# Performance work log

Hardware: AMD Instinct MI355X
Metric: run time of the kernel (lower is better)

The kernel has to match this reference:

```python
import jax, jax.numpy as jnp
import numpy as np

B, S, D, FF, E = 4, 2048, 2048, 8192, 2


def setup_inputs() -> dict:
    key = jax.random.key(0)
    k0, k1, k2, k3, k4 = jax.random.split(key, 5)
    s = 0.02  # init scale for weights
    return {
        "hidden_states": jax.random.normal(k0, (B, S, D), jnp.float32),
        "gate_w": jax.random.normal(k1, (E, D), jnp.float32) * s,   # router Linear weight
        "w_gate": jax.random.normal(k2, (E, FF, D), jnp.float32) * s,  # per-expert gate_proj
        "w_up": jax.random.normal(k3, (E, FF, D), jnp.float32) * s,    # per-expert up_proj
        "w_down": jax.random.normal(k4, (E, D, FF), jnp.float32) * s,  # per-expert down_proj
    }


def reference(hidden_states, gate_w, w_gate, w_up, w_down):
    b, s, d = hidden_states.shape
    x = hidden_states.reshape(-1, d)                      # [T, D], T = B*S
    logits = x @ gate_w.T                                  # [T, E]
    probs = jax.nn.softmax(logits.astype(jnp.float32), axis=-1)
    sel = jnp.argmax(probs, axis=-1)                       # top-1 expert per token
    top_w = jnp.take_along_axis(probs, sel[:, None], axis=-1)  # [T, 1] routing weight
    onehot = jax.nn.one_hot(sel, gate_w.shape[0], dtype=x.dtype)  # [T, E]
    # Dense per-expert MistralMLP: down(silu(gate(x)) * up(x)); top-1 combine via one-hot mask.
    g = jnp.einsum('td,efd->etf', x, w_gate)               # [E, T, FF]
    u = jnp.einsum('td,efd->etf', x, w_up)                 # [E, T, FF]
    h = jax.nn.silu(g) * u
    y = jnp.einsum('etf,edf->etd', h, w_down)              # [E, T, D]
    out = jnp.einsum('etd,te->td', y, onehot * top_w)      # weighted scatter-combine
    return out.reshape(b, s, d)
```

## Files before the change

kernel.cpp:

```cpp
#include <hip/hip_runtime.h>
#include <hip/hip_bf16.h>

#define T_TOK   8192
#define D_DIM   2048
#define FF_DIM  8192
#define PADT    8448

#define C_CNT0 0
#define C_CNT1 1
#define C_CUR0 2
#define C_BASE1 4
#define C_PTOT 5

typedef __attribute__((ext_vector_type(4))) float f32x4;
typedef __attribute__((ext_vector_type(8))) short short8;

__device__ __forceinline__ unsigned short f2bf(float f) {
  union { __hip_bfloat16 b; unsigned short u; } cv;
  cv.b = __float2bfloat16(f);
  return cv.u;
}

__device__ __forceinline__ void gload16(const void* g, void* l) {
  __builtin_amdgcn_global_load_lds(
      (const __attribute__((address_space(1))) void*)g,
      (__attribute__((address_space(3))) void*)l,
      16, 0, 0);
}

__global__ __launch_bounds__(256) void cvt_kernel(const float4* __restrict__ src,
                                                  ushort4* __restrict__ dst, int n4) {
  int i = blockIdx.x * blockDim.x + threadIdx.x;
  if (i < n4) {
    float4 v = src[i];
    dst[i] = make_ushort4(f2bf(v.x), f2bf(v.y), f2bf(v.z), f2bf(v.w));
  }
}

__global__ __launch_bounds__(256) void init_kernel(int* __restrict__ ctrl,
                                                   int* __restrict__ perm) {
  int i = blockIdx.x * blockDim.x + threadIdx.x;
  if (i < 8) ctrl[i] = 0;
  if (i < PADT) perm[i] = -1;
}

__global__ __launch_bounds__(256) void router_kernel(const float* __restrict__ x,
                                                     const float* __restrict__ gw,
                                                     int* __restrict__ sel,
                                                     float* __restrict__ topw,
                                                     int* __restrict__ ctrl) {
  const int w = threadIdx.x >> 6, l = threadIdx.x & 63;
  const int t = blockIdx.x * 4 + w;
  const float4* xr = (const float4*)(x + (size_t)t * D_DIM);
  const float4* g0 = (const float4*)gw;
  const float4* g1 = (const float4*)(gw + D_DIM);
  float d0 = 0.f, d1 = 0.f;
#pragma unroll
  for (int i = 0; i < 8; i++) {
    float4 v = xr[i * 64 + l];
    float4 a = g0[i * 64 + l];
    float4 b = g1[i * 64 + l];
    d0 += v.x * a.x + v.y * a.y + v.z * a.z + v.w * a.w;
    d1 += v.x * b.x + v.y * b.y + v.z * b.z + v.w * b.w;
  }
#pragma unroll
  for (int s = 32; s; s >>= 1) {
    d0 += __shfl_xor(d0, s);
    d1 += __shfl_xor(d1, s);
  }
  if (l == 0) {
    int e = (d1 > d0) ? 1 : 0;
    float dd = fabsf(d1 - d0);
    sel[t] = e;
    topw[t] = 1.f / (1.f + expf(-dd));
    atomicAdd(&ctrl[e], 1);
  }
}

__global__ void setup_kernel(int* __restrict__ ctrl) {
  if (threadIdx.x == 0) {
    int c0 = ctrl[C_CNT0], c1 = ctrl[C_CNT1];
    int b1 = ((c0 + 127) >> 7) << 7;
    ctrl[C_BASE1] = b1;
    ctrl[C_PTOT] = b1 + (((c1 + 127) >> 7) << 7);
  }
}

__global__ __launch_bounds__(256) void scatter_kernel(const int* __restrict__ sel,
                                                      int* __restrict__ ctrl,
                                                      int* __restrict__ perm) {
  int t = blockIdx.x * blockDim.x + threadIdx.x;
  int e = sel[t];
  int base = e ? ctrl[C_BASE1] : 0;
  int pos = base + atomicAdd(&ctrl[C_CUR0 + e], 1);
  perm[pos] = t;
}

__global__ __launch_bounds__(256) void gather_kernel(const float* __restrict__ x,
                                                     const int* __restrict__ perm,
                                                     const float* __restrict__ topw,
                                                     ushort* __restrict__ Xg,
                                                     float* __restrict__ twg) {
  const int w = threadIdx.x >> 6, l = threadIdx.x & 63;
  const int pos = blockIdx.x * 4 + w;
  const int t = perm[pos];
  if (l == 0) twg[pos] = (t >= 0) ? topw[t] : 0.f;
  ushort4* dst = (ushort4*)(Xg + (size_t)pos * D_DIM);
  if (t >= 0) {
    const float4* src = (const float4*)(x + (size_t)t * D_DIM);
#pragma unroll
    for (int i = 0; i < 8; i++) {
      float4 v = src[i * 64 + l];
      dst[i * 64 + l] = make_ushort4(f2bf(v.x), f2bf(v.y), f2bf(v.z), f2bf(v.w));
    }
  } else {
    ushort4 z = make_ushort4(0, 0, 0, 0);
#pragma unroll
    for (int i = 0; i < 8; i++) dst[i * 64 + l] = z;
  }
}

__global__ __launch_bounds__(256, 2) void gemm1_kernel(const ushort* __restrict__ Xg,
                                                       const ushort* __restrict__ Wg,
                                                       const ushort* __restrict__ Wu,
                                                       ushort* __restrict__ H,
                                                       const int* __restrict__ ctrl) {
  __shared__ ushort As[128 * 32];
  __shared__ ushort Bgs[128 * 32];
  __shared__ ushort Bus[128 * 32];

  const int row0 = blockIdx.x * 128;
  if (row0 >= ctrl[C_PTOT]) return;
  const int e = (row0 >= ctrl[C_BASE1]) ? 1 : 0;
  const int tn = blockIdx.y;

  const int tid = threadIdx.x;
  const int w = tid >> 6, l = tid & 63;
  const int wr = w >> 1, wc = w & 1;

  const ushort* A  = Xg + (size_t)row0 * D_DIM;
  const ushort* Bg = Wg + ((size_t)e * FF_DIM + (size_t)tn * 128) * D_DIM;
  const ushort* Bu = Wu + ((size_t)e * FF_DIM + (size_t)tn * 128) * D_DIM;

  const int q0 = w * 2, q1 = q0 + 1;
  const int scol = (l & 3) * 8;
  const ushort* a0  = A  + (size_t)(q0 * 16 + (l >> 2)) * D_DIM + scol;
  const ushort* a1  = A  + (size_t)(q1 * 16 + (l >> 2)) * D_DIM + scol;
  const ushort* bg0 = Bg + (size_t)(q0 * 16 + (l >> 2)) * D_DIM + scol;
  const ushort* bg1 = Bg + (size_t)(q1 * 16 + (l >> 2)) * D_DIM + scol;
  const ushort* bu0 = Bu + (size_t)(q0 * 16 + (l >> 2)) * D_DIM + scol;
  const ushort* bu1 = Bu + (size_t)(q1 * 16 + (l >> 2)) * D_DIM + scol;
  ushort* lA0 = &As [q0 * 512];
  ushort* lA1 = &As [q1 * 512];
  ushort* lG0 = &Bgs[q0 * 512];
  ushort* lG1 = &Bgs[q1 * 512];
  ushort* lU0 = &Bus[q0 * 512];
  ushort* lU1 = &Bus[q1 * 512];

  f32x4 accg[4][4] = {};
  f32x4 accu[4][4] = {};

  const int fr = l & 15, fk = (l >> 4) * 8;

  for (int k0 = 0; k0 < D_DIM; k0 += 32) {
    gload16(a0 + k0, lA0);
    gload16(a1 + k0, lA1);
    gload16(bg0 + k0, lG0);
    gload16(bg1 + k0, lG1);
    gload16(bu0 + k0, lU0);
    gload16(bu1 + k0, lU1);
    __syncthreads();
    short8 a[4], bg[4], bu[4];
#pragma unroll
    for (int i = 0; i < 4; i++) a[i]  = *(const short8*)&As [(wr * 64 + i * 16 + fr) * 32 + fk];
#pragma unroll
    for (int j = 0; j < 4; j++) bg[j] = *(const short8*)&Bgs[(wc * 64 + j * 16 + fr) * 32 + fk];
#pragma unroll
    for (int j = 0; j < 4; j++) bu[j] = *(const short8*)&Bus[(wc * 64 + j * 16 + fr) * 32 + fk];
#pragma unroll
    for (int i = 0; i < 4; i++)
#pragma unroll
      for (int j = 0; j < 4; j++) {
        accg[i][j] = __builtin_amdgcn_mfma_f32_16x16x32_bf16(a[i], bg[j], accg[i][j], 0, 0, 0);
        accu[i][j] = __builtin_amdgcn_mfma_f32_16x16x32_bf16(a[i], bu[j], accu[i][j], 0, 0, 0);
      }
    __syncthreads();
  }

  const int m4 = (l >> 4) * 4;
#pragma unroll
  for (int i = 0; i < 4; i++) {
#pragma unroll
    for (int r = 0; r < 4; r++) {
      size_t hrow = (size_t)(row0 + wr * 64 + i * 16 + m4 + r) * FF_DIM + (size_t)tn * 128 + wc * 64;
#pragma unroll
      for (int j = 0; j < 4; j++) {
        float g = accg[i][j][r], u = accu[i][j][r];
        float h = (g / (1.f + __expf(-g))) * u;
        H[hrow + j * 16 + fr] = f2bf(h);
      }
    }
  }
}

__global__ __launch_bounds__(256, 2) void gemm2_kernel(const ushort* __restrict__ H,
                                                       const ushort* __restrict__ Wd,
                                                       const int* __restrict__ perm,
                                                       const float* __restrict__ twg,
                                                       float* __restrict__ out,
                                                       const int* __restrict__ ctrl) {
  __shared__ ushort As[128 * 32];
  __shared__ ushort Bs[128 * 32];

  const int row0 = blockIdx.x * 128;
  if (row0 >= ctrl[C_PTOT]) return;
  const int e = (row0 >= ctrl[C_BASE1]) ? 1 : 0;
  const int tn = blockIdx.y;

  const int tid = threadIdx.x;
  const int w = tid >> 6, l = tid & 63;
  const int wr = w >> 1, wc = w & 1;

  const ushort* A = H  + (size_t)row0 * FF_DIM;
  const ushort* B = Wd + ((size_t)e * D_DIM + (size_t)tn * 128) * FF_DIM;

  const int q0 = w * 2, q1 = q0 + 1;
  const int scol = (l & 3) * 8;
  const ushort* a0 = A + (size_t)(q0 * 16 + (l >> 2)) * FF_DIM + scol;
  const ushort* a1 = A + (size_t)(q1 * 16 + (l >> 2)) * FF_DIM + scol;
  const ushort* b0 = B + (size_t)(q0 * 16 + (l >> 2)) * FF_DIM + scol;
  const ushort* b1 = B + (size_t)(q1 * 16 + (l >> 2)) * FF_DIM + scol;
  ushort* lA0 = &As[q0 * 512];
  ushort* lA1 = &As[q1 * 512];
  ushort* lB0 = &Bs[q0 * 512];
  ushort* lB1 = &Bs[q1 * 512];

  f32x4 acc[4][4] = {};
  const int fr = l & 15, fk = (l >> 4) * 8;

  for (int k0 = 0; k0 < FF_DIM; k0 += 32) {
    gload16(a0 + k0, lA0);
    gload16(a1 + k0, lA1);
    gload16(b0 + k0, lB0);
    gload16(b1 + k0, lB1);
    __syncthreads();
    short8 a[4], b[4];
#pragma unroll
    for (int i = 0; i < 4; i++) a[i] = *(const short8*)&As[(wr * 64 + i * 16 + fr) * 32 + fk];
#pragma unroll
    for (int j = 0; j < 4; j++) b[j] = *(const short8*)&Bs[(wc * 64 + j * 16 + fr) * 32 + fk];
#pragma unroll
    for (int i = 0; i < 4; i++)
#pragma unroll
      for (int j = 0; j < 4; j++)
        acc[i][j] = __builtin_amdgcn_mfma_f32_16x16x32_bf16(a[i], b[j], acc[i][j], 0, 0, 0);
    __syncthreads();
  }

  const int m4 = (l >> 4) * 4;
#pragma unroll
  for (int i = 0; i < 4; i++) {
#pragma unroll
    for (int r = 0; r < 4; r++) {
      int prow = row0 + wr * 64 + i * 16 + m4 + r;
      int tok = perm[prow];
      if (tok < 0) continue;
      float tw = twg[prow];
      float* orow = out + (size_t)tok * D_DIM + (size_t)tn * 128 + wc * 64;
#pragma unroll
      for (int j = 0; j < 4; j++) orow[j * 16 + fr] = acc[i][j][r] * tw;
    }
  }
}

extern "C" void kernel_launch(void* const* d_in, const int* in_sizes, int n_in,
                              void* d_out, int out_size, void* d_ws, size_t ws_size,
                              hipStream_t stream) {
  const float* x  = (const float*)d_in[0];
  const float* gw = (const float*)d_in[1];
  const float* wg = (const float*)d_in[2];
  const float* wu = (const float*)d_in[3];
  const float* wd = (const float*)d_in[4];
  float* out = (float*)d_out;

  char* ws = (char*)d_ws;
  size_t off = 0;
  auto alloc = [&](size_t bytes) -> void* {
    void* p = ws + off;
    off += (bytes + 255) & ~(size_t)255;
    return p;
  };
  const size_t WELEM = (size_t)2 * FF_DIM * D_DIM;
  ushort* Wg_b = (ushort*)alloc(WELEM * 2);
  ushort* Wu_b = (ushort*)alloc(WELEM * 2);
  ushort* Wd_b = (ushort*)alloc(WELEM * 2);
  ushort* Xg   = (ushort*)alloc((size_t)PADT * D_DIM * 2);
  ushort* Hbuf = (ushort*)alloc((size_t)PADT * FF_DIM * 2);
  int*   sel  = (int*)alloc(T_TOK * 4);
  float* topw = (float*)alloc(T_TOK * 4);
  int*   perm = (int*)alloc(PADT * 4);
  float* twg  = (float*)alloc(PADT * 4);
  int*   ctrl = (int*)alloc(256);
  (void)ws_size; (void)in_sizes; (void)n_in; (void)out_size;

  const int n4 = (int)(WELEM / 4);
  cvt_kernel<<<n4 / 256, 256, 0, stream>>>((const float4*)wg, (ushort4*)Wg_b, n4);
  cvt_kernel<<<n4 / 256, 256, 0, stream>>>((const float4*)wu, (ushort4*)Wu_b, n4);
  cvt_kernel<<<n4 / 256, 256, 0, stream>>>((const float4*)wd, (ushort4*)Wd_b, n4);

  init_kernel<<<(PADT + 255) / 256, 256, 0, stream>>>(ctrl, perm);
  router_kernel<<<T_TOK / 4, 256, 0, stream>>>(x, gw, sel, topw, ctrl);
  setup_kernel<<<1, 64, 0, stream>>>(ctrl);
  scatter_kernel<<<T_TOK / 256, 256, 0, stream>>>(sel, ctrl, perm);
  gather_kernel<<<PADT / 4, 256, 0, stream>>>(x, perm, topw, Xg, twg);

  dim3 g1(PADT / 128, FF_DIM / 128);
  gemm1_kernel<<<g1, 256, 0, stream>>>(Xg, Wg_b, Wu_b, Hbuf, ctrl);
  dim3 g2(PADT / 128, D_DIM / 128);
  gemm2_kernel<<<g2, 256, 0, stream>>>(Hbuf, Wd_b, perm, twg, out, ctrl);
}
```

Measured before the change: 1.969 ms.

## Rewrite expert GEMMs with 256-row tiles, triple-buffered LDS pipeline and grid swizzle

Both expert GEMMs move to 512-thread blocks with 256x128 (gemm1, gate/up interleaved) and 256x256 (gemm2) output tiles. K-slices are staged through a three-deep LDS ring with XOR-swizzled layout, using vmcnt-based waits instead of full syncthreads. Block IDs are swizzled for L2 locality, and the three weight-conversion launches are merged into one grid-stride kernel. Expert padding grows to 256 rows to match the tile, which adds some wasted compute. The larger tiles also raise register and LDS pressure.

```diff
diff --git a/kernel.cpp b/kernel.cpp
--- a/kernel.cpp
+++ b/kernel.cpp
@@ -5,6 +5,11 @@
 #define D_DIM   2048
 #define FF_DIM  8192
 #define PADT    8448
+#define NMT     33
+#define G1_GRID (NMT*64)
+#define G2_GRID (NMT*8)
+#define NT1     64
+#define NT2     256
 
 #define C_CNT0 0
 #define C_CNT1 1
@@ -28,12 +33,20 @@
       16, 0, 0);
 }
 
-__global__ __launch_bounds__(256) void cvt_kernel(const float4* __restrict__ src,
-                                                  ushort4* __restrict__ dst, int n4) {
-  int i = blockIdx.x * blockDim.x + threadIdx.x;
-  if (i < n4) {
-    float4 v = src[i];
-    dst[i] = make_ushort4(f2bf(v.x), f2bf(v.y), f2bf(v.z), f2bf(v.w));
+__global__ __launch_bounds__(256) void cvt3_kernel(const float4* __restrict__ sa,
+                                                   const float4* __restrict__ sb,
+                                                   const float4* __restrict__ sc,
+                                                   ushort4* __restrict__ da,
+                                                   ushort4* __restrict__ db,
+                                                   ushort4* __restrict__ dc, int n4) {
+  const int stride = gridDim.x * blockDim.x;
+  for (int i = blockIdx.x * blockDim.x + threadIdx.x; i < n4; i += stride) {
+    float4 v = sa[i];
+    da[i] = make_ushort4(f2bf(v.x), f2bf(v.y), f2bf(v.z), f2bf(v.w));
+    v = sb[i];
+    db[i] = make_ushort4(f2bf(v.x), f2bf(v.y), f2bf(v.z), f2bf(v.w));
+    v = sc[i];
+    dc[i] = make_ushort4(f2bf(v.x), f2bf(v.y), f2bf(v.z), f2bf(v.w));
   }
 }
 
@@ -80,9 +93,9 @@
 __global__ void setup_kernel(int* __restrict__ ctrl) {
   if (threadIdx.x == 0) {
     int c0 = ctrl[C_CNT0], c1 = ctrl[C_CNT1];
-    int b1 = ((c0 + 127) >> 7) << 7;
+    int b1 = ((c0 + 255) >> 8) << 8;
     ctrl[C_BASE1] = b1;
-    ctrl[C_PTOT] = b1 + (((c1 + 127) >> 7) << 7);
+    ctrl[C_PTOT] = b1 + (((c1 + 255) >> 8) << 8);
   }
 }
 
@@ -120,153 +133,182 @@
   }
 }
 
-__global__ __launch_bounds__(256, 2) void gemm1_kernel(const ushort* __restrict__ Xg,
+
+__global__ __launch_bounds__(512, 2) void gemm1_kernel(const ushort* __restrict__ Xg,
                                                        const ushort* __restrict__ Wg,
                                                        const ushort* __restrict__ Wu,
                                                        ushort* __restrict__ H,
                                                        const int* __restrict__ ctrl) {
-  __shared__ ushort As[128 * 32];
-  __shared__ ushort Bgs[128 * 32];
-  __shared__ ushort Bus[128 * 32];
-
-  const int row0 = blockIdx.x * 128;
-  if (row0 >= ctrl[C_PTOT]) return;
+  __shared__ ushort lds[3 * 16384];
+  const int ptot = ctrl[C_PTOT];
+  const int bid = blockIdx.x;
+  const int swz = (bid & 7) * (G1_GRID / 8) + (bid >> 3);
+  const int tn = swz / NMT, bx = swz % NMT;
+  const int row0 = bx * 256;
+  if (row0 >= ptot) return;
   const int e = (row0 >= ctrl[C_BASE1]) ? 1 : 0;
-  const int tn = blockIdx.y;
-
-  const int tid = threadIdx.x;
-  const int w = tid >> 6, l = tid & 63;
-  const int wr = w >> 1, wc = w & 1;
-
-  const ushort* A  = Xg + (size_t)row0 * D_DIM;
-  const ushort* Bg = Wg + ((size_t)e * FF_DIM + (size_t)tn * 128) * D_DIM;
-  const ushort* Bu = Wu + ((size_t)e * FF_DIM + (size_t)tn * 128) * D_DIM;
-
-  const int q0 = w * 2, q1 = q0 + 1;
-  const int scol = (l & 3) * 8;
-  const ushort* a0  = A  + (size_t)(q0 * 16 + (l >> 2)) * D_DIM + scol;
-  const ushort* a1  = A  + (size_t)(q1 * 16 + (l >> 2)) * D_DIM + scol;
-  const ushort* bg0 = Bg + (size_t)(q0 * 16 + (l >> 2)) * D_DIM + scol;
-  const ushort* bg1 = Bg + (size_t)(q1 * 16 + (l >> 2)) * D_DIM + scol;
-  const ushort* bu0 = Bu + (size_t)(q0 * 16 + (l >> 2)) * D_DIM + scol;
-  const ushort* bu1 = Bu + (size_t)(q1 * 16 + (l >> 2)) * D_DIM + scol;
-  ushort* lA0 = &As [q0 * 512];
-  ushort* lA1 = &As [q1 * 512];
-  ushort* lG0 = &Bgs[q0 * 512];
-  ushort* lG1 = &Bgs[q1 * 512];
-  ushort* lU0 = &Bus[q0 * 512];
-  ushort* lU1 = &Bus[q1 * 512];
-
-  f32x4 accg[4][4] = {};
-  f32x4 accu[4][4] = {};
-
-  const int fr = l & 15, fk = (l >> 4) * 8;
-
-  for (int k0 = 0; k0 < D_DIM; k0 += 32) {
-    gload16(a0 + k0, lA0);
-    gload16(a1 + k0, lA1);
-    gload16(bg0 + k0, lG0);
-    gload16(bg1 + k0, lG1);
-    gload16(bu0 + k0, lU0);
-    gload16(bu1 + k0, lU1);
-    __syncthreads();
-    short8 a[4], bg[4], bu[4];
-#pragma unroll
-    for (int i = 0; i < 4; i++) a[i]  = *(const short8*)&As [(wr * 64 + i * 16 + fr) * 32 + fk];
-#pragma unroll
-    for (int j = 0; j < 4; j++) bg[j] = *(const short8*)&Bgs[(wc * 64 + j * 16 + fr) * 32 + fk];
-#pragma unroll
-    for (int j = 0; j < 4; j++) bu[j] = *(const short8*)&Bus[(wc * 64 + j * 16 + fr) * 32 + fk];
-#pragma unroll
-    for (int i = 0; i < 4; i++)
-#pragma unroll
-      for (int j = 0; j < 4; j++) {
-        accg[i][j] = __builtin_amdgcn_mfma_f32_16x16x32_bf16(a[i], bg[j], accg[i][j], 0, 0, 0);
-        accu[i][j] = __builtin_amdgcn_mfma_f32_16x16x32_bf16(a[i], bu[j], accu[i][j], 0, 0, 0);
+
+  const int tid = threadIdx.x, w = tid >> 6, l = tid & 63;
+  const int wr = w >> 2, wc = w & 3;
+  const int fr = l & 15, kg = l >> 4;
+
+  auto srcptr = [&](int li) -> const ushort* {
+    int o = li * 8192 + w * 1024 + l * 16;
+    int row = o >> 7, pc = (o >> 4) & 7;
+    int lc = pc ^ (row & 7);
+    if (lc < 4)
+      return Xg + (size_t)(row0 + row) * D_DIM + lc * 8;
+    int mat = (row >> 4) & 1;
+    int ff = tn * 128 + ((row >> 5) << 4) + (row & 15);
+    return (mat ? Wu : Wg) + ((size_t)e * FF_DIM + ff) * D_DIM + (lc - 4) * 8;
+  };
+  const ushort* s0 = srcptr(0);
+  const ushort* s1 = srcptr(1);
+  const ushort* s2 = srcptr(2);
+  const ushort* s3 = srcptr(3);
+
+  auto STAGE = [&](int buf) {
+    ushort* db = lds + buf * 16384 + (w << 9);
+    gload16(s0, db);          s0 += 32;
+    gload16(s1, db + 4096);   s1 += 32;
+    gload16(s2, db + 8192);   s2 += 32;
+    gload16(s3, db + 12288);  s3 += 32;
+  };
+
+  const int aoff = (wr * 128 + fr) * 128 + ((kg ^ (fr & 7)) << 4);
+  const int boff = (wc * 64 + fr) * 128 + (((4 ^ kg) ^ (fr & 7)) << 4);
+
+  f32x4 acc[8][4] = {};
+
+  STAGE(0);
+  STAGE(1);
+  int sbuf = 2, cbuf = 0;
+  for (int t = 0; t < NT1; ++t) {
+    if (t < NT1 - 1) asm volatile("s_waitcnt vmcnt(4)" ::: "memory");
+    else             asm volatile("s_waitcnt vmcnt(0)" ::: "memory");
+    __builtin_amdgcn_s_barrier();
+    asm volatile("" ::: "memory");
+    if (t + 2 < NT1) {
+      STAGE(sbuf);
+      sbuf = (sbuf == 2) ? 0 : sbuf + 1;
+    }
+    const char* Lb = (const char*)lds + cbuf * 32768;
+    cbuf = (cbuf == 2) ? 0 : cbuf + 1;
+    short8 bfrag[4], afrag[8];
+#pragma unroll
+    for (int j = 0; j < 4; j++) bfrag[j] = *(const short8*)(Lb + boff + j * 2048);
+#pragma unroll
+    for (int i = 0; i < 8; i++) afrag[i] = *(const short8*)(Lb + aoff + i * 2048);
+    __builtin_amdgcn_s_setprio(1);
+#pragma unroll
+    for (int i = 0; i < 8; i++)
+#pragma unroll
+      for (int j = 0; j < 4; j++)
+        acc[i][j] = __builtin_amdgcn_mfma_f32_16x16x32_bf16(afrag[i], bfrag[j], acc[i][j], 0, 0, 0);
+    __builtin_amdgcn_s_setprio(0);
+    asm volatile("" ::: "memory");
+  }
+
+  const int m4 = kg * 4;
+#pragma unroll
+  for (int i = 0; i < 8; i++) {
+#pragma unroll
+    for (int r = 0; r < 4; r++) {
+      size_t hbase = (size_t)(row0 + wr * 128 + i * 16 + m4 + r) * FF_DIM;
+#pragma unroll
+      for (int p = 0; p < 2; p++) {
+        float g = acc[i][2 * p][r], u = acc[i][2 * p + 1][r];
+        float h = (g / (1.f + __expf(-g))) * u;
+        H[hbase + tn * 128 + (wc * 2 + p) * 16 + fr] = f2bf(h);
       }
-    __syncthreads();
-  }
-
-  const int m4 = (l >> 4) * 4;
-#pragma unroll
-  for (int i = 0; i < 4; i++) {
-#pragma unroll
-    for (int r = 0; r < 4; r++) {
-      size_t hrow = (size_t)(row0 + wr * 64 + i * 16 + m4 + r) * FF_DIM + (size_t)tn * 128 + wc * 64;
-#pragma unroll
-      for (int j = 0; j < 4; j++) {
-        float g = accg[i][j][r], u = accu[i][j][r];
-        float h = (g / (1.f + __expf(-g))) * u;
-        H[hrow + j * 16 + fr] = f2bf(h);
-      }
-    }
-  }
-}
-
-__global__ __launch_bounds__(256, 2) void gemm2_kernel(const ushort* __restrict__ H,
+    }
+  }
+}
+
+__global__ __launch_bounds__(512, 2) void gemm2_kernel(const ushort* __restrict__ Hb,
                                                        const ushort* __restrict__ Wd,
                                                        const int* __restrict__ perm,
                                                        const float* __restrict__ twg,
                                                        float* __restrict__ out,
                                                        const int* __restrict__ ctrl) {
-  __shared__ ushort As[128 * 32];
-  __shared__ ushort Bs[128 * 32];
-
-  const int row0 = blockIdx.x * 128;
-  if (row0 >= ctrl[C_PTOT]) return;
+  __shared__ ushort lds[3 * 16384];
+  const int ptot = ctrl[C_PTOT];
+  const int bid = blockIdx.x;
+  const int swz = (bid & 7) * (G2_GRID / 8) + (bid >> 3);
+  const int tn = swz / NMT, bx = swz % NMT;
+  const int row0 = bx * 256;
+  if (row0 >= ptot) return;
   const int e = (row0 >= ctrl[C_BASE1]) ? 1 : 0;
-  const int tn = blockIdx.y;
-
-  const int tid = threadIdx.x;
-  const int w = tid >> 6, l = tid & 63;
-  const int wr = w >> 1, wc = w & 1;
-
-  const ushort* A = H  + (size_t)row0 * FF_DIM;
-  const ushort* B = Wd + ((size_t)e * D_DIM + (size_t)tn * 128) * FF_DIM;
-
-  const int q0 = w * 2, q1 = q0 + 1;
-  const int scol = (l & 3) * 8;
-  const ushort* a0 = A + (size_t)(q0 * 16 + (l >> 2)) * FF_DIM + scol;
-  const ushort* a1 = A + (size_t)(q1 * 16 + (l >> 2)) * FF_DIM + scol;
-  const ushort* b0 = B + (size_t)(q0 * 16 + (l >> 2)) * FF_DIM + scol;
-  const ushort* b1 = B + (size_t)(q1 * 16 + (l >> 2)) * FF_DIM + scol;
-  ushort* lA0 = &As[q0 * 512];
-  ushort* lA1 = &As[q1 * 512];
-  ushort* lB0 = &Bs[q0 * 512];
-  ushort* lB1 = &Bs[q1 * 512];
-
-  f32x4 acc[4][4] = {};
-  const int fr = l & 15, fk = (l >> 4) * 8;
-
-  for (int k0 = 0; k0 < FF_DIM; k0 += 32) {
-    gload16(a0 + k0, lA0);
-    gload16(a1 + k0, lA1);
-    gload16(b0 + k0, lB0);
-    gload16(b1 + k0, lB1);
-    __syncthreads();
-    short8 a[4], b[4];
-#pragma unroll
-    for (int i = 0; i < 4; i++) a[i] = *(const short8*)&As[(wr * 64 + i * 16 + fr) * 32 + fk];
-#pragma unroll
-    for (int j = 0; j < 4; j++) b[j] = *(const short8*)&Bs[(wc * 64 + j * 16 + fr) * 32 + fk];
-#pragma unroll
-    for (int i = 0; i < 4; i++)
+
+  const int tid = threadIdx.x, w = tid >> 6, l = tid & 63;
+  const int wr = w >> 2, wc = w & 3;
+  const int fr = l & 15, kg = l >> 4;
+
+  auto srcptr = [&](int li) -> const ushort* {
+    int o = li * 8192 + w * 1024 + l * 16;
+    int row = o >> 7, pc = (o >> 4) & 7;
+    int lc = pc ^ (row & 7);
+    if (lc < 4)
+      return Hb + (size_t)(row0 + row) * FF_DIM + lc * 8;
+    return Wd + ((size_t)e * D_DIM + tn * 256 + row) * FF_DIM + (lc - 4) * 8;
+  };
+  const ushort* s0 = srcptr(0);
+  const ushort* s1 = srcptr(1);
+  const ushort* s2 = srcptr(2);
+  const ushort* s3 = srcptr(3);
+
+  auto STAGE = [&](int buf) {
+    ushort* db = lds + buf * 16384 + (w << 9);
+    gload16(s0, db);          s0 += 32;
+    gload16(s1, db + 4096);   s1 += 32;
+    gload16(s2, db + 8192);   s2 += 32;
+    gload16(s3, db + 12288);  s3 += 32;
+  };
+
+  const int aoff = (wr * 128 + fr) * 128 + ((kg ^ (fr & 7)) << 4);
+  const int boff = (wc * 64 + fr) * 128 + (((4 ^ kg) ^ (fr & 7)) << 4);
+
+  f32x4 acc[8][4] = {};
+
+  STAGE(0);
+  STAGE(1);
+  int sbuf = 2, cbuf = 0;
+  for (int t = 0; t < NT2; ++t) {
+    if (t < NT2 - 1) asm volatile("s_waitcnt vmcnt(4)" ::: "memory");
+    else             asm volatile("s_waitcnt vmcnt(0)" ::: "memory");
+    __builtin_amdgcn_s_barrier();
+    asm volatile("" ::: "memory");
+    if (t + 2 < NT2) {
+      STAGE(sbuf);
+      sbuf = (sbuf == 2) ? 0 : sbuf + 1;
+    }
+    const char* Lb = (const char*)lds + cbuf * 32768;
+    cbuf = (cbuf == 2) ? 0 : cbuf + 1;
+    short8 bfrag[4], afrag[8];
+#pragma unroll
+    for (int j = 0; j < 4; j++) bfrag[j] = *(const short8*)(Lb + boff + j * 2048);
+#pragma unroll
+    for (int i = 0; i < 8; i++) afrag[i] = *(const short8*)(Lb + aoff + i * 2048);
+    __builtin_amdgcn_s_setprio(1);
+#pragma unroll
+    for (int i = 0; i < 8; i++)
 #pragma unroll
       for (int j = 0; j < 4; j++)
-        acc[i][j] = __builtin_amdgcn_mfma_f32_16x16x32_bf16(a[i], b[j], acc[i][j], 0, 0, 0);
-    __syncthreads();
-  }
-
-  const int m4 = (l >> 4) * 4;
-#pragma unroll
-  for (int i = 0; i < 4; i++) {
+        acc[i][j] = __builtin_amdgcn_mfma_f32_16x16x32_bf16(afrag[i], bfrag[j], acc[i][j], 0, 0, 0);
+    __builtin_amdgcn_s_setprio(0);
+    asm volatile("" ::: "memory");
+  }
+
+  const int m4 = kg * 4;
+#pragma unroll
+  for (int i = 0; i < 8; i++) {
 #pragma unroll
     for (int r = 0; r < 4; r++) {
-      int prow = row0 + wr * 64 + i * 16 + m4 + r;
+      int prow = row0 + wr * 128 + i * 16 + m4 + r;
       int tok = perm[prow];
       if (tok < 0) continue;
       float tw = twg[prow];
-      float* orow = out + (size_t)tok * D_DIM + (size_t)tn * 128 + wc * 64;
+      float* orow = out + (size_t)tok * D_DIM + tn * 256 + wc * 64;
 #pragma unroll
       for (int j = 0; j < 4; j++) orow[j * 16 + fr] = acc[i][j][r] * tw;
     }
@@ -304,9 +346,9 @@
   (void)ws_size; (void)in_sizes; (void)n_in; (void)out_size;
 
   const int n4 = (int)(WELEM / 4);
-  cvt_kernel<<<n4 / 256, 256, 0, stream>>>((const float4*)wg, (ushort4*)Wg_b, n4);
-  cvt_kernel<<<n4 / 256, 256, 0, stream>>>((const float4*)wu, (ushort4*)Wu_b, n4);
-  cvt_kernel<<<n4 / 256, 256, 0, stream>>>((const float4*)wd, (ushort4*)Wd_b, n4);
+  cvt3_kernel<<<4096, 256, 0, stream>>>((const float4*)wg, (const float4*)wu,
+                                        (const float4*)wd, (ushort4*)Wg_b,
+                                        (ushort4*)Wu_b, (ushort4*)Wd_b, n4);
 
   init_kernel<<<(PADT + 255) / 256, 256, 0, stream>>>(ctrl, perm);
   router_kernel<<<T_TOK / 4, 256, 0, stream>>>(x, gw, sel, topw, ctrl);
@@ -314,8 +356,6 @@
   scatter_kernel<<<T_TOK / 256, 256, 0, stream>>>(sel, ctrl, perm);
   gather_kernel<<<PADT / 4, 256, 0, stream>>>(x, perm, topw, Xg, twg);
 
-  dim3 g1(PADT / 128, FF_DIM / 128);
-  gemm1_kernel<<<g1, 256, 0, stream>>>(Xg, Wg_b, Wu_b, Hbuf, ctrl);
-  dim3 g2(PADT / 128, D_DIM / 128);
-  gemm2_kernel<<<g2, 256, 0, stream>>>(Hbuf, Wd_b, perm, twg, out, ctrl);
-}
+  gemm1_kernel<<<G1_GRID, 512, 0, stream>>>(Xg, Wg_b, Wu_b, Hbuf, ctrl);
+  gemm2_kernel<<<G2_GRID, 512, 0, stream>>>(Hbuf, Wd_b, perm, twg, out, ctrl);
+}
```

Result: faster. 1.649 ms (-16.2%).
